# Performance work log

Hardware: AMD Instinct MI355X
Metric: run time of the kernel (lower is better)

The kernel has to match this reference:

```python
import jax, jax.numpy as jnp
import numpy as np

N_NODES = 100000
N_EDGES = 1600000
IN_DIM = 128
HID_DIM = 128


def setup_inputs() -> dict:
    key = jax.random.key(0)
    k_x, k_e, k_w1, k_w2 = jax.random.split(key, 4)
    x = jax.random.normal(k_x, (N_NODES, IN_DIM), dtype=jnp.float32)
    edge_index = jax.random.randint(k_e, (2, N_EDGES), 0, N_NODES, dtype=jnp.int64)
    # Glorot-style init like PyG GCNConv
    s1 = 1.0 / np.sqrt(IN_DIM)
    s2 = 1.0 / np.sqrt(HID_DIM)
    W1 = jax.random.uniform(k_w1, (IN_DIM, HID_DIM), jnp.float32, -s1, s1)
    b1 = jnp.zeros((HID_DIM,), jnp.float32)
    W2 = jax.random.uniform(k_w2, (HID_DIM, HID_DIM), jnp.float32, -s2, s2)
    b2 = jnp.zeros((HID_DIM,), jnp.float32)
    return {"x": x, "edge_index": edge_index, "W1": W1, "b1": b1, "W2": W2, "b2": b2}


def _gcn_norm(edge_index, num_nodes):
    # add self-loops, then symmetric normalization D^{-1/2} (A+I) D^{-1/2}
    loops = jnp.arange(num_nodes, dtype=edge_index.dtype)
    src = jnp.concatenate([edge_index[0], loops])
    dst = jnp.concatenate([edge_index[1], loops])
    deg = jax.ops.segment_sum(jnp.ones_like(dst, dtype=jnp.float32), dst,
                              num_segments=num_nodes)
    dinv = jnp.where(deg > 0, jax.lax.rsqrt(deg), 0.0)
    norm = dinv[src] * dinv[dst]  # [E + N]
    return src, dst, norm


def _gcn_conv(x, W, b, src, dst, norm, num_nodes):
    h = x @ W  # transform first (out_dim == in_dim here, order matches PyG)
    msg = h[src] * norm[:, None]  # gather + scale, [E+N, D]
    out = jax.ops.segment_sum(msg, dst, num_segments=num_nodes)
    return out + b


def reference(x, edge_index, W1, b1, W2, b2):
    n = x.shape[0]
    src, dst, norm = _gcn_norm(edge_index, n)
    h = _gcn_conv(x, W1, b1, src, dst, norm, n)
    h = jax.nn.relu(h)
    return _gcn_conv(h, W2, b2, src, dst, norm, n)
```

## Files before the change

### kernel.cpp

```cpp
#include <hip/hip_runtime.h>
#include <hip/hip_bf16.h>


#define LHSZ 800
#define MAXB 4096
#define CAP  2560

typedef unsigned int uint;
typedef unsigned short ushort;
typedef __attribute__((ext_vector_type(8))) short bf16x8;
typedef __attribute__((ext_vector_type(4))) float f32x4;

static __device__ __forceinline__ float bfl(uint u) { return __uint_as_float(u << 16); }
static __device__ __forceinline__ float bfh(uint u) { return __uint_as_float(u & 0xffff0000u); }
static __device__ __forceinline__ ushort f2bfu(float f) {
    __hip_bfloat16 b = __float2bfloat16(f);
    ushort u; __builtin_memcpy(&u, &b, 2); return u;
}
static __device__ __forceinline__ void splitT(float f, ushort& h, ushort& l) {
    uint u = __float_as_uint(f);
    h = (ushort)(u >> 16);
    float r = f - __uint_as_float(u & 0xffff0000u);
    l = (ushort)(__float_as_uint(r) >> 16);
}

__global__ __launch_bounds__(256) void wsplit_init(
    const float* __restrict__ W1, const float* __restrict__ W2,
    ushort* __restrict__ Ws1, ushort* __restrict__ Ws2,
    int* __restrict__ cur, int nb)
{
    int tg = blockIdx.x * 256 + threadIdx.x;
    int w = tg >> 14;
    int e = tg & 16383;
    int k = e >> 7, n = e & 127;
    float f = (w ? W2 : W1)[e];
    ushort hi, lo; splitT(f, hi, lo);
    int I = (n * 128 + k) ^ ((n & 7) << 3);
    ushort* o = w ? Ws2 : Ws1;
    o[I] = hi; o[I + 16384] = lo;
    if (tg < nb) cur[tg] = tg * CAP;
}

template <int MODE>
static __device__ __forceinline__ void gemm_body(
    ushort* Wt, const void* __restrict__ Ap, const ushort* __restrict__ Wsp,
    ushort* __restrict__ out, int M, int blk)
{
    int t = threadIdx.x;
    {
        const uint4* s4 = (const uint4*)Wsp;
        uint4* d4 = (uint4*)Wt;
        #pragma unroll
        for (int j = 0; j < 16; ++j)
            d4[t + j * 256] = s4[t + j * 256];
    }
    __syncthreads();

    int wv = t >> 6, lane = t & 63;
    int g = lane >> 4;
    int lr = lane & 15;
    int rowbase = blk * 128 + wv * 32;
    int r0 = rowbase + lr, r1 = r0 + 16;
    int rc0 = min(r0, M - 1), rc1 = min(r1, M - 1);

    f32x4 acc[2][8];
    #pragma unroll
    for (int rt = 0; rt < 2; ++rt)
        #pragma unroll
        for (int ct = 0; ct < 8; ++ct)
            acc[rt][ct] = (f32x4)0.0f;

    #pragma unroll
    for (int ks = 0; ks < 4; ++ks) {
        int kof = ks * 32 + g * 8;
        bf16x8 ahi[2], alo[2];
        if (MODE == 0) {
            const float* A = (const float*)Ap;
            #pragma unroll
            for (int rt = 0; rt < 2; ++rt) {
                const float4* p = (const float4*)(A + (size_t)(rt ? rc1 : rc0) * 128 + kof);
                float4 u0 = p[0], u1 = p[1];
                float uu[8] = {u0.x, u0.y, u0.z, u0.w, u1.x, u1.y, u1.z, u1.w};
                bf16x8 ah, al;
                #pragma unroll
                for (int q = 0; q < 8; ++q) {
                    ushort hh, ll; splitT(uu[q], hh, ll);
                    ah[q] = (short)hh; al[q] = (short)ll;
                }
                ahi[rt] = ah; alo[rt] = al;
            }
        } else {
            const ushort* A = (const ushort*)Ap;
            ahi[0] = *(const bf16x8*)(A + (size_t)rc0 * 128 + kof);
            ahi[1] = *(const bf16x8*)(A + (size_t)rc1 * 128 + kof);
        }
        #pragma unroll
        for (int ct = 0; ct < 8; ++ct) {
            int n = ct * 16 + lr;
            int I = (n * 128 + kof) ^ ((n & 7) << 3);
            bf16x8 bhi = *(const bf16x8*)&Wt[I];
            bf16x8 blo = *(const bf16x8*)&Wt[I + 16384];
            #pragma unroll
            for (int rt = 0; rt < 2; ++rt) {
                acc[rt][ct] = __builtin_amdgcn_mfma_f32_16x16x32_bf16(ahi[rt], bhi, acc[rt][ct], 0, 0, 0);
                acc[rt][ct] = __builtin_amdgcn_mfma_f32_16x16x32_bf16(ahi[rt], blo, acc[rt][ct], 0, 0, 0);
                if (MODE == 0)
                    acc[rt][ct] = __builtin_amdgcn_mfma_f32_16x16x32_bf16(alo[rt], bhi, acc[rt][ct], 0, 0, 0);
            }
        }
    }

    #pragma unroll
    for (int rt = 0; rt < 2; ++rt) {
        #pragma unroll
        for (int r = 0; r < 4; ++r) {
            int row = rowbase + rt * 16 + g * 4 + r;
            if (row < M) {
                #pragma unroll
                for (int ct = 0; ct < 8; ++ct)
                    out[(size_t)row * 128 + ct * 16 + lr] = f2bfu(acc[rt][ct][r]);
            }
        }
    }
}

template <int MODE>
__global__ __launch_bounds__(256) void gemm_mfma(
    const void* __restrict__ Ap, const ushort* __restrict__ Wsp,
    ushort* __restrict__ out, int M)
{
    __shared__ ushort Wt[2 * 128 * 128];
    gemm_body<MODE>(Wt, Ap, Wsp, out, M, blockIdx.x);
}

__global__ __launch_bounds__(256) void gemm1_place(
    const float* __restrict__ x, const ushort* __restrict__ Wsp,
    ushort* __restrict__ h, int M, int gemmGrid,
    const int* __restrict__ src, const int* __restrict__ dst,
    int* __restrict__ cur, uint* __restrict__ ppack, int E, int nb, int epb)
{
    __shared__ ushort Wt[2 * 128 * 128];
    if ((int)blockIdx.x >= gemmGrid) {
        int* lhist = (int*)Wt;
        int* gb    = lhist + LHSZ;
        int b = blockIdx.x - gemmGrid;
        int t = threadIdx.x;
        int e0 = b * epb, e1 = min(E, e0 + epb);
        for (int i = t; i < nb; i += 256) lhist[i] = 0;
        __syncthreads();
        for (int e = e0 + t; e < e1; e += 256) atomicAdd(&lhist[dst[e] >> 7], 1);
        __syncthreads();
        for (int i = t; i < nb; i += 256) {
            int v = lhist[i];
            gb[i] = v ? atomicAdd(&cur[i], v) : 0;
            lhist[i] = 0;
        }
        __syncthreads();
        for (int e = e0 + t; e < e1; e += 256) {
            int d = dst[e];
            int b2 = d >> 7;
            int r = atomicAdd(&lhist[b2], 1);
            int pos = gb[b2] + r;
            if (pos < (b2 + 1) * CAP)
                ppack[pos] = (uint)src[e] | ((uint)(d & 127) << 20);
        }
        return;
    }
    gemm_body<0>(Wt, x, Wsp, h, M, blockIdx.x);
}

__global__ __launch_bounds__(256) void csr_finalize(
    const uint* __restrict__ ppack, const int* __restrict__ cur,
    int* __restrict__ csrsrc, uint* __restrict__ meta,
    float* __restrict__ dinv, int N)
{
    __shared__ int ncnt[128], sbuf[128], ncur[128];
    __shared__ int srcbuf[MAXB];
    int t = threadIdx.x;
    int b = blockIdx.x;
    int node0 = b << 7;
    int nn = min(128, N - node0);
    int base = b * CAP;
    int len = min(cur[b] - base, CAP);

    if (t < 128) ncnt[t] = 0;
    __syncthreads();
    for (int i = t; i < len; i += 256)
        atomicAdd(&ncnt[ppack[base + i] >> 20], 1);
    __syncthreads();
    if (t < 128) sbuf[t] = ncnt[t];
    __syncthreads();
    for (int d = 1; d < 128; d <<= 1) {
        int v = 0;
        if (t < 128 && t >= d) v = sbuf[t - d];
        __syncthreads();
        if (t < 128) sbuf[t] += v;
        __syncthreads();
    }
    if (t < 128) {
        int excl = sbuf[t] - ncnt[t];
        ncur[t] = excl;
        if (t < nn) {
            meta[node0 + t] = ((uint)(base + excl) << 10) | (uint)min(ncnt[t], 1023);
            dinv[node0 + t] = rsqrtf((float)(ncnt[t] + 1));
        }
    }
    __syncthreads();
    bool staged = (len <= MAXB);
    for (int i = t; i < len; i += 256) {
        uint p = ppack[base + i];
        int pos = atomicAdd(&ncur[p >> 20], 1);
        int sl = (int)(p & 0xFFFFFu);
        if (staged) srcbuf[pos] = sl;
        else        csrsrc[base + pos] = sl;
    }
    __syncthreads();
    if (staged)
        for (int i = t; i < len; i += 256) csrsrc[base + i] = srcbuf[i];
}

#define FMA4(v, wgt) do { float wf_ = (wgt); \
    acc.x += bfl((v).x) * wf_; acc.y += bfh((v).x) * wf_; \
    acc.z += bfl((v).y) * wf_; acc.w += bfh((v).y) * wf_; } while (0)

template <bool RELU, bool OUTBF>
__global__ __launch_bounds__(256) void agg_kernel(
    const ushort* __restrict__ h, const float* __restrict__ dinv,
    const uint* __restrict__ meta, const int* __restrict__ csrsrc,
    const float* __restrict__ bias, void* __restrict__ outv, int n)
{
    __shared__ int2 epair[4][64];
    int wv = threadIdx.x >> 6;
    int lane = threadIdx.x & 63;
    int half = lane >> 5, sub = lane & 31;
    int node = (blockIdx.x * 4 + wv) * 2 + half;
    bool active = node < n;
    int nodeC = active ? node : (n - 1);

    const uint2* h2 = (const uint2*)h;
    float di = dinv[nodeC];
    uint md = meta[nodeC];
    int beg = (int)(md >> 10);
    int m = (int)(md & 1023u);

    uint2 vs = h2[(size_t)nodeC * 32 + sub];
    float w0 = di * di;
    float4 acc;
    acc.x = bfl(vs.x) * w0; acc.y = bfh(vs.x) * w0;
    acc.z = bfl(vs.y) * w0; acc.w = bfh(vs.y) * w0;

    int mA = __shfl(m, 0), mB = __shfl(m, 32);
    int mmax = max(mA, mB);

    for (int eb = 0; eb < mmax; eb += 32) {
        int sl = 0; float dlw = 0.0f;
        if (active && (eb + sub) < m) {
            sl = csrsrc[beg + eb + sub];
            dlw = di * dinv[sl];
        }
        epair[wv][lane] = make_int2(sl, __float_as_int(dlw));
        int nq = mmax - eb; if (nq > 32) nq = 32;
        const int2* ep = &epair[wv][half * 32];
        for (int j = 0; j < nq; j += 4) {
            int2 p0 = ep[j + 0];
            int2 p1 = ep[j + 1];
            int2 p2 = ep[j + 2];
            int2 p3 = ep[j + 3];
            uint2 v0 = h2[(size_t)(uint)p0.x * 32 + sub];
            uint2 v1 = h2[(size_t)(uint)p1.x * 32 + sub];
            uint2 v2 = h2[(size_t)(uint)p2.x * 32 + sub];
            uint2 v3 = h2[(size_t)(uint)p3.x * 32 + sub];
            FMA4(v0, __int_as_float(p0.y));
            FMA4(v1, __int_as_float(p1.y));
            FMA4(v2, __int_as_float(p2.y));
            FMA4(v3, __int_as_float(p3.y));
        }
    }

    float4 bb = ((const float4*)bias)[sub];
    acc.x += bb.x; acc.y += bb.y; acc.z += bb.z; acc.w += bb.w;
    if (RELU) {
        acc.x = fmaxf(acc.x, 0.0f); acc.y = fmaxf(acc.y, 0.0f);
        acc.z = fmaxf(acc.z, 0.0f); acc.w = fmaxf(acc.w, 0.0f);
    }
    if (active) {
        if (OUTBF) {
            uint2 o;
            o.x = (uint)f2bfu(acc.x) | ((uint)f2bfu(acc.y) << 16);
            o.y = (uint)f2bfu(acc.z) | ((uint)f2bfu(acc.w) << 16);
            ((uint2*)outv)[(size_t)node * 32 + sub] = o;
        } else {
            ((float4*)outv)[(size_t)node * 32 + sub] = acc;
        }
    }
}

extern "C" void kernel_launch(void* const* d_in, const int* in_sizes, int n_in,
                              void* d_out, int out_size, void* d_ws, size_t ws_size,
                              hipStream_t stream)
{
    const float* x  = (const float*)d_in[0];
    const int*   ei = (const int*)d_in[1];
    const float* W1 = (const float*)d_in[2];
    const float* b1 = (const float*)d_in[3];
    const float* W2 = (const float*)d_in[4];
    const float* b2 = (const float*)d_in[5];

    const int N = in_sizes[0] / 128;
    const int E = in_sizes[1] / 2;
    const int* esrc = ei;
    const int* edst = ei + E;
    const int nb = (N + 127) >> 7;

    char* ws = (char*)d_ws;
    size_t off = 0;
    auto alloc = [&](size_t bytes) -> void* {
        void* p = ws + off;
        off += (bytes + 255) & ~(size_t)255;
        return p;
    };
    ushort* h      = (ushort*)alloc((size_t)N * 128 * sizeof(ushort));
    uint*   ppack  = (uint*)  alloc((size_t)nb * CAP * sizeof(uint));
    int*    csrsrc = (int*)   alloc((size_t)nb * CAP * sizeof(int));
    uint*   meta   = (uint*)  alloc((size_t)N * sizeof(uint));
    float*  dinv   = (float*) alloc((size_t)N * sizeof(float));
    int*    cur    = (int*)   alloc((size_t)nb * sizeof(int));
    ushort* Ws1    = (ushort*)alloc(2 * 128 * 128 * sizeof(ushort));
    ushort* Ws2    = (ushort*)alloc(2 * 128 * 128 * sizeof(ushort));

    const int gridP = 512;
    const int epb = (E + gridP - 1) / gridP;
    const int gemmGrid = (N + 127) / 128;

    wsplit_init<<<128, 256, 0, stream>>>(W1, W2, Ws1, Ws2, cur, nb);
    gemm1_place<<<gemmGrid + gridP, 256, 0, stream>>>(x, Ws1, h, N, gemmGrid,
                                                      esrc, edst, cur, ppack,
                                                      E, nb, epb);
    csr_finalize<<<nb, 256, 0, stream>>>(ppack, cur, csrsrc, meta, dinv, N);
    agg_kernel<true, true><<<(N + 7) / 8, 256, 0, stream>>>(h, dinv, meta, csrsrc,
                                                            b1, d_out, N);
    gemm_mfma<1><<<gemmGrid, 256, 0, stream>>>(d_out, Ws2, h, N);
    agg_kernel<false, false><<<(N + 7) / 8, 256, 0, stream>>>(h, dinv, meta, csrsrc,
                                                              b2, d_out, N);
}
```

Baseline: 195.1 us.

## Fuse CSR finalize into aggregation using per-bucket shared-memory edge lists

Removes the separate csr_finalize kernel and the csrsrc/meta/dinv arrays. Each aggregation block of 1024 threads now re-sorts its 128-node bucket from ppack into shared memory and computes per-edge weights from a global degree array. That degree array is built with atomics during the placement pass. This saves a launch and a global CSR round trip, but the bucket sort and the per-edge rsqrt are redone in both aggregation layers, global degree atomics are added, and there is less parallelism per block.

```diff
diff --git a/kernel.cpp b/kernel.cpp
--- a/kernel.cpp
+++ b/kernel.cpp
@@ -3,7 +3,6 @@
 
 
 #define LHSZ 800
-#define MAXB 4096
 #define CAP  2560
 
 typedef unsigned int uint;
@@ -24,10 +23,10 @@
     l = (ushort)(__float_as_uint(r) >> 16);
 }
 
-__global__ __launch_bounds__(256) void wsplit_init(
+__global__ __launch_bounds__(256) void init_all(
     const float* __restrict__ W1, const float* __restrict__ W2,
     ushort* __restrict__ Ws1, ushort* __restrict__ Ws2,
-    int* __restrict__ cur, int nb)
+    int* __restrict__ deg, int* __restrict__ cur, int N, int nb)
 {
     int tg = blockIdx.x * 256 + threadIdx.x;
     int w = tg >> 14;
@@ -38,6 +37,7 @@
     int I = (n * 128 + k) ^ ((n & 7) << 3);
     ushort* o = w ? Ws2 : Ws1;
     o[I] = hi; o[I + 16384] = lo;
+    for (int i = tg; i < N; i += 32768) deg[i] = 0;
     if (tg < nb) cur[tg] = tg * CAP;
 }
 
@@ -137,7 +137,8 @@
     const float* __restrict__ x, const ushort* __restrict__ Wsp,
     ushort* __restrict__ h, int M, int gemmGrid,
     const int* __restrict__ src, const int* __restrict__ dst,
-    int* __restrict__ cur, uint* __restrict__ ppack, int E, int nb, int epb)
+    int* __restrict__ cur, int* __restrict__ deg,
+    uint* __restrict__ ppack, int E, int nb, int epb)
 {
     __shared__ ushort Wt[2 * 128 * 128];
     if ((int)blockIdx.x >= gemmGrid) {
@@ -148,7 +149,11 @@
         int e0 = b * epb, e1 = min(E, e0 + epb);
         for (int i = t; i < nb; i += 256) lhist[i] = 0;
         __syncthreads();
-        for (int e = e0 + t; e < e1; e += 256) atomicAdd(&lhist[dst[e] >> 7], 1);
+        for (int e = e0 + t; e < e1; e += 256) {
+            int d = dst[e];
+            atomicAdd(&lhist[d >> 7], 1);
+            atomicAdd(&deg[d], 1);
+        }
         __syncthreads();
         for (int i = t; i < nb; i += 256) {
             int v = lhist[i];
@@ -169,24 +174,34 @@
     gemm_body<0>(Wt, x, Wsp, h, M, blockIdx.x);
 }
 
-__global__ __launch_bounds__(256) void csr_finalize(
+#define FMA4(v, wgt) do { float wf_ = (wgt); \
+    acc.x += bfl((v).x) * wf_; acc.y += bfh((v).x) * wf_; \
+    acc.z += bfl((v).y) * wf_; acc.w += bfh((v).y) * wf_; } while (0)
+
+template <bool RELU, bool OUTBF>
+__global__ __launch_bounds__(1024) void agg_fused(
+    const ushort* __restrict__ h, const int* __restrict__ deg,
     const uint* __restrict__ ppack, const int* __restrict__ cur,
-    int* __restrict__ csrsrc, uint* __restrict__ meta,
-    float* __restrict__ dinv, int N)
-{
+    const float* __restrict__ bias, void* __restrict__ outv, int n)
+{
+    __shared__ int   lsrc[CAP];
+    __shared__ float lwt[CAP];
     __shared__ int ncnt[128], sbuf[128], ncur[128];
-    __shared__ int srcbuf[MAXB];
+    __shared__ float dloc[128];
     int t = threadIdx.x;
     int b = blockIdx.x;
     int node0 = b << 7;
-    int nn = min(128, N - node0);
     int base = b * CAP;
     int len = min(cur[b] - base, CAP);
 
     if (t < 128) ncnt[t] = 0;
     __syncthreads();
-    for (int i = t; i < len; i += 256)
-        atomicAdd(&ncnt[ppack[base + i] >> 20], 1);
+    uint myp[3]; int mc = 0;
+    for (int i = t; i < len; i += 1024) {
+        uint p = ppack[base + i];
+        myp[mc++] = p;
+        atomicAdd(&ncnt[p >> 20], 1);
+    }
     __syncthreads();
     if (t < 128) sbuf[t] = ncnt[t];
     __syncthreads();
@@ -198,99 +213,75 @@
         __syncthreads();
     }
     if (t < 128) {
-        int excl = sbuf[t] - ncnt[t];
-        ncur[t] = excl;
-        if (t < nn) {
-            meta[node0 + t] = ((uint)(base + excl) << 10) | (uint)min(ncnt[t], 1023);
-            dinv[node0 + t] = rsqrtf((float)(ncnt[t] + 1));
-        }
-    }
-    __syncthreads();
-    bool staged = (len <= MAXB);
-    for (int i = t; i < len; i += 256) {
-        uint p = ppack[base + i];
+        ncur[t] = sbuf[t] - ncnt[t];
+        dloc[t] = rsqrtf((float)(ncnt[t] + 1));
+    }
+    __syncthreads();
+    for (int k = 0; k < mc; ++k) {
+        uint p = myp[k];
         int pos = atomicAdd(&ncur[p >> 20], 1);
-        int sl = (int)(p & 0xFFFFFu);
-        if (staged) srcbuf[pos] = sl;
-        else        csrsrc[base + pos] = sl;
-    }
-    __syncthreads();
-    if (staged)
-        for (int i = t; i < len; i += 256) csrsrc[base + i] = srcbuf[i];
-}
-
-#define FMA4(v, wgt) do { float wf_ = (wgt); \
-    acc.x += bfl((v).x) * wf_; acc.y += bfh((v).x) * wf_; \
-    acc.z += bfl((v).y) * wf_; acc.w += bfh((v).y) * wf_; } while (0)
-
-template <bool RELU, bool OUTBF>
-__global__ __launch_bounds__(256) void agg_kernel(
-    const ushort* __restrict__ h, const float* __restrict__ dinv,
-    const uint* __restrict__ meta, const int* __restrict__ csrsrc,
-    const float* __restrict__ bias, void* __restrict__ outv, int n)
-{
-    __shared__ int2 epair[4][64];
-    int wv = threadIdx.x >> 6;
-    int lane = threadIdx.x & 63;
+        lsrc[pos] = (int)(p & 0xFFFFFu);
+    }
+    __syncthreads();
+    for (int i = t; i < len; i += 1024)
+        lwt[i] = rsqrtf((float)(deg[lsrc[i]] + 1));
+    __syncthreads();
+
+    int wv = t >> 6, lane = t & 63;
     int half = lane >> 5, sub = lane & 31;
-    int node = (blockIdx.x * 4 + wv) * 2 + half;
-    bool active = node < n;
-    int nodeC = active ? node : (n - 1);
-
     const uint2* h2 = (const uint2*)h;
-    float di = dinv[nodeC];
-    uint md = meta[nodeC];
-    int beg = (int)(md >> 10);
-    int m = (int)(md & 1023u);
-
-    uint2 vs = h2[(size_t)nodeC * 32 + sub];
-    float w0 = di * di;
-    float4 acc;
-    acc.x = bfl(vs.x) * w0; acc.y = bfh(vs.x) * w0;
-    acc.z = bfl(vs.y) * w0; acc.w = bfh(vs.y) * w0;
-
-    int mA = __shfl(m, 0), mB = __shfl(m, 32);
-    int mmax = max(mA, mB);
-
-    for (int eb = 0; eb < mmax; eb += 32) {
-        int sl = 0; float dlw = 0.0f;
-        if (active && (eb + sub) < m) {
-            sl = csrsrc[beg + eb + sub];
-            dlw = di * dinv[sl];
-        }
-        epair[wv][lane] = make_int2(sl, __float_as_int(dlw));
-        int nq = mmax - eb; if (nq > 32) nq = 32;
-        const int2* ep = &epair[wv][half * 32];
-        for (int j = 0; j < nq; j += 4) {
-            int2 p0 = ep[j + 0];
-            int2 p1 = ep[j + 1];
-            int2 p2 = ep[j + 2];
-            int2 p3 = ep[j + 3];
-            uint2 v0 = h2[(size_t)(uint)p0.x * 32 + sub];
-            uint2 v1 = h2[(size_t)(uint)p1.x * 32 + sub];
-            uint2 v2 = h2[(size_t)(uint)p2.x * 32 + sub];
-            uint2 v3 = h2[(size_t)(uint)p3.x * 32 + sub];
-            FMA4(v0, __int_as_float(p0.y));
-            FMA4(v1, __int_as_float(p1.y));
-            FMA4(v2, __int_as_float(p2.y));
-            FMA4(v3, __int_as_float(p3.y));
-        }
-    }
-
-    float4 bb = ((const float4*)bias)[sub];
-    acc.x += bb.x; acc.y += bb.y; acc.z += bb.z; acc.w += bb.w;
-    if (RELU) {
-        acc.x = fmaxf(acc.x, 0.0f); acc.y = fmaxf(acc.y, 0.0f);
-        acc.z = fmaxf(acc.z, 0.0f); acc.w = fmaxf(acc.w, 0.0f);
-    }
-    if (active) {
-        if (OUTBF) {
-            uint2 o;
-            o.x = (uint)f2bfu(acc.x) | ((uint)f2bfu(acc.y) << 16);
-            o.y = (uint)f2bfu(acc.z) | ((uint)f2bfu(acc.w) << 16);
-            ((uint2*)outv)[(size_t)node * 32 + sub] = o;
-        } else {
-            ((float4*)outv)[(size_t)node * 32 + sub] = acc;
+
+    for (int pp = 0; pp < 4; ++pp) {
+        int ln = pp * 32 + wv * 2 + half;
+        int node = node0 + ln;
+        bool active = node < n;
+        int nodeC = active ? node : (n - 1);
+        float di = dloc[ln];
+        int m = ncnt[ln];
+        int beg = ncur[ln] - m;
+
+        uint2 vs = h2[(size_t)nodeC * 32 + sub];
+        float4 acc = make_float4(0.0f, 0.0f, 0.0f, 0.0f);
+
+        int j = 0;
+        for (; j + 4 <= m; j += 4) {
+            int s0 = lsrc[beg + j + 0], s1 = lsrc[beg + j + 1];
+            int s2 = lsrc[beg + j + 2], s3 = lsrc[beg + j + 3];
+            float q0 = lwt[beg + j + 0], q1 = lwt[beg + j + 1];
+            float q2 = lwt[beg + j + 2], q3 = lwt[beg + j + 3];
+            uint2 v0 = h2[(size_t)(uint)s0 * 32 + sub];
+            uint2 v1 = h2[(size_t)(uint)s1 * 32 + sub];
+            uint2 v2 = h2[(size_t)(uint)s2 * 32 + sub];
+            uint2 v3 = h2[(size_t)(uint)s3 * 32 + sub];
+            FMA4(v0, q0); FMA4(v1, q1); FMA4(v2, q2); FMA4(v3, q3);
+        }
+        for (; j < m; ++j) {
+            int s0 = lsrc[beg + j];
+            float q0 = lwt[beg + j];
+            uint2 v0 = h2[(size_t)(uint)s0 * 32 + sub];
+            FMA4(v0, q0);
+        }
+
+        float w0 = di * di;
+        acc.x = acc.x * di + bfl(vs.x) * w0;
+        acc.y = acc.y * di + bfh(vs.x) * w0;
+        acc.z = acc.z * di + bfl(vs.y) * w0;
+        acc.w = acc.w * di + bfh(vs.y) * w0;
+        float4 bb = ((const float4*)bias)[sub];
+        acc.x += bb.x; acc.y += bb.y; acc.z += bb.z; acc.w += bb.w;
+        if (RELU) {
+            acc.x = fmaxf(acc.x, 0.0f); acc.y = fmaxf(acc.y, 0.0f);
+            acc.z = fmaxf(acc.z, 0.0f); acc.w = fmaxf(acc.w, 0.0f);
+        }
+        if (active) {
+            if (OUTBF) {
+                uint2 o;
+                o.x = (uint)f2bfu(acc.x) | ((uint)f2bfu(acc.y) << 16);
+                o.y = (uint)f2bfu(acc.z) | ((uint)f2bfu(acc.w) << 16);
+                ((uint2*)outv)[(size_t)node * 32 + sub] = o;
+            } else {
+                ((float4*)outv)[(size_t)node * 32 + sub] = acc;
+            }
         }
     }
 }
@@ -321,9 +312,7 @@
     };
     ushort* h      = (ushort*)alloc((size_t)N * 128 * sizeof(ushort));
     uint*   ppack  = (uint*)  alloc((size_t)nb * CAP * sizeof(uint));
-    int*    csrsrc = (int*)   alloc((size_t)nb * CAP * sizeof(int));
-    uint*   meta   = (uint*)  alloc((size_t)N * sizeof(uint));
-    float*  dinv   = (float*) alloc((size_t)N * sizeof(float));
+    int*    deg    = (int*)   alloc((size_t)N * sizeof(int));
     int*    cur    = (int*)   alloc((size_t)nb * sizeof(int));
     ushort* Ws1    = (ushort*)alloc(2 * 128 * 128 * sizeof(ushort));
     ushort* Ws2    = (ushort*)alloc(2 * 128 * 128 * sizeof(ushort));
@@ -332,14 +321,13 @@
     const int epb = (E + gridP - 1) / gridP;
     const int gemmGrid = (N + 127) / 128;
 
-    wsplit_init<<<128, 256, 0, stream>>>(W1, W2, Ws1, Ws2, cur, nb);
+    init_all<<<128, 256, 0, stream>>>(W1, W2, Ws1, Ws2, deg, cur, N, nb);
     gemm1_place<<<gemmGrid + gridP, 256, 0, stream>>>(x, Ws1, h, N, gemmGrid,
-                                                      esrc, edst, cur, ppack,
-                                                      E, nb, epb);
-    csr_finalize<<<nb, 256, 0, stream>>>(ppack, cur, csrsrc, meta, dinv, N);
-    agg_kernel<true, true><<<(N + 7) / 8, 256, 0, stream>>>(h, dinv, meta, csrsrc,
-                                                            b1, d_out, N);
+                                                      esrc, edst, cur, deg,
+                                                      ppack, E, nb, epb);
+    agg_fused<true, true><<<nb, 1024, 0, stream>>>(h, deg, ppack, cur,
+                                                   b1, d_out, N);
     gemm_mfma<1><<<gemmGrid, 256, 0, stream>>>(d_out, Ws2, h, N);
-    agg_kernel<false, false><<<(N + 7) / 8, 256, 0, stream>>>(h, dinv, meta, csrsrc,
-                                                              b2, d_out, N);
-}
+    agg_fused<false, false><<<nb, 1024, 0, stream>>>(h, deg, ppack, cur,
+                                                     b2, d_out, N);
+}
```

After: 271.9 us. 39.4% more time.

## Co-schedule CSR finalize with first GEMM instead of bucket placement

Applied to the files above, without the earlier changes.

Moves edge bucket placement into its own small kernel and merges the CSR finalize step into the first GEMM launch as extra blocks. The finalize blocks then overlap with GEMM blocks rather than running as a separate serial launch. Placement loses its overlap with the GEMM, and finalize blocks now occupy the GEMM kernel's 64KB LDS allocation, which may lower occupancy for those blocks.

```diff
diff --git a/kernel.cpp b/kernel.cpp
--- a/kernel.cpp
+++ b/kernel.cpp
@@ -39,6 +39,85 @@
     ushort* o = w ? Ws2 : Ws1;
     o[I] = hi; o[I + 16384] = lo;
     if (tg < nb) cur[tg] = tg * CAP;
+}
+
+__global__ __launch_bounds__(256) void bucket_place(
+    const int* __restrict__ src, const int* __restrict__ dst,
+    int* __restrict__ cur, uint* __restrict__ ppack, int E, int nb, int epb)
+{
+    __shared__ int lhist[LHSZ];
+    __shared__ int gb[LHSZ];
+    int t = threadIdx.x;
+    int e0 = blockIdx.x * epb, e1 = min(E, e0 + epb);
+    for (int i = t; i < nb; i += 256) lhist[i] = 0;
+    __syncthreads();
+    for (int e = e0 + t; e < e1; e += 256) atomicAdd(&lhist[dst[e] >> 7], 1);
+    __syncthreads();
+    for (int i = t; i < nb; i += 256) {
+        int v = lhist[i];
+        gb[i] = v ? atomicAdd(&cur[i], v) : 0;
+        lhist[i] = 0;
+    }
+    __syncthreads();
+    for (int e = e0 + t; e < e1; e += 256) {
+        int d = dst[e];
+        int b2 = d >> 7;
+        int r = atomicAdd(&lhist[b2], 1);
+        int pos = gb[b2] + r;
+        if (pos < (b2 + 1) * CAP)
+            ppack[pos] = (uint)src[e] | ((uint)(d & 127) << 20);
+    }
+}
+
+static __device__ __forceinline__ void finalize_body(
+    char* lds, const uint* __restrict__ ppack, const int* __restrict__ cur,
+    int* __restrict__ csrsrc, uint* __restrict__ meta,
+    float* __restrict__ dinv, int N, int b)
+{
+    int* ncnt  = (int*)lds;
+    int* sbuf  = ncnt + 128;
+    int* ncur  = sbuf + 128;
+    int* srcbuf = ncur + 128;
+    int t = threadIdx.x;
+    int node0 = b << 7;
+    int nn = min(128, N - node0);
+    int base = b * CAP;
+    int len = min(cur[b] - base, CAP);
+
+    if (t < 128) ncnt[t] = 0;
+    __syncthreads();
+    for (int i = t; i < len; i += 256)
+        atomicAdd(&ncnt[ppack[base + i] >> 20], 1);
+    __syncthreads();
+    if (t < 128) sbuf[t] = ncnt[t];
+    __syncthreads();
+    for (int d = 1; d < 128; d <<= 1) {
+        int v = 0;
+        if (t < 128 && t >= d) v = sbuf[t - d];
+        __syncthreads();
+        if (t < 128) sbuf[t] += v;
+        __syncthreads();
+    }
+    if (t < 128) {
+        int excl = sbuf[t] - ncnt[t];
+        ncur[t] = excl;
+        if (t < nn) {
+            meta[node0 + t] = ((uint)(base + excl) << 10) | (uint)min(ncnt[t], 1023);
+            dinv[node0 + t] = rsqrtf((float)(ncnt[t] + 1));
+        }
+    }
+    __syncthreads();
+    bool staged = (len <= MAXB);
+    for (int i = t; i < len; i += 256) {
+        uint p = ppack[base + i];
+        int pos = atomicAdd(&ncur[p >> 20], 1);
+        int sl = (int)(p & 0xFFFFFu);
+        if (staged) srcbuf[pos] = sl;
+        else        csrsrc[base + pos] = sl;
+    }
+    __syncthreads();
+    if (staged)
+        for (int i = t; i < len; i += 256) csrsrc[base + i] = srcbuf[i];
 }
 
 template <int MODE>
@@ -133,90 +212,20 @@
     gemm_body<MODE>(Wt, Ap, Wsp, out, M, blockIdx.x);
 }
 
-__global__ __launch_bounds__(256) void gemm1_place(
+__global__ __launch_bounds__(256) void gemm1_fin(
     const float* __restrict__ x, const ushort* __restrict__ Wsp,
     ushort* __restrict__ h, int M, int gemmGrid,
-    const int* __restrict__ src, const int* __restrict__ dst,
-    int* __restrict__ cur, uint* __restrict__ ppack, int E, int nb, int epb)
-{
-    __shared__ ushort Wt[2 * 128 * 128];
-    if ((int)blockIdx.x >= gemmGrid) {
-        int* lhist = (int*)Wt;
-        int* gb    = lhist + LHSZ;
-        int b = blockIdx.x - gemmGrid;
-        int t = threadIdx.x;
-        int e0 = b * epb, e1 = min(E, e0 + epb);
-        for (int i = t; i < nb; i += 256) lhist[i] = 0;
-        __syncthreads();
-        for (int e = e0 + t; e < e1; e += 256) atomicAdd(&lhist[dst[e] >> 7], 1);
-        __syncthreads();
-        for (int i = t; i < nb; i += 256) {
-            int v = lhist[i];
-            gb[i] = v ? atomicAdd(&cur[i], v) : 0;
-            lhist[i] = 0;
-        }
-        __syncthreads();
-        for (int e = e0 + t; e < e1; e += 256) {
-            int d = dst[e];
-            int b2 = d >> 7;
-            int r = atomicAdd(&lhist[b2], 1);
-            int pos = gb[b2] + r;
-            if (pos < (b2 + 1) * CAP)
-                ppack[pos] = (uint)src[e] | ((uint)(d & 127) << 20);
-        }
-        return;
-    }
-    gemm_body<0>(Wt, x, Wsp, h, M, blockIdx.x);
-}
-
-__global__ __launch_bounds__(256) void csr_finalize(
     const uint* __restrict__ ppack, const int* __restrict__ cur,
     int* __restrict__ csrsrc, uint* __restrict__ meta,
     float* __restrict__ dinv, int N)
 {
-    __shared__ int ncnt[128], sbuf[128], ncur[128];
-    __shared__ int srcbuf[MAXB];
-    int t = threadIdx.x;
-    int b = blockIdx.x;
-    int node0 = b << 7;
-    int nn = min(128, N - node0);
-    int base = b * CAP;
-    int len = min(cur[b] - base, CAP);
-
-    if (t < 128) ncnt[t] = 0;
-    __syncthreads();
-    for (int i = t; i < len; i += 256)
-        atomicAdd(&ncnt[ppack[base + i] >> 20], 1);
-    __syncthreads();
-    if (t < 128) sbuf[t] = ncnt[t];
-    __syncthreads();
-    for (int d = 1; d < 128; d <<= 1) {
-        int v = 0;
-        if (t < 128 && t >= d) v = sbuf[t - d];
-        __syncthreads();
-        if (t < 128) sbuf[t] += v;
-        __syncthreads();
-    }
-    if (t < 128) {
-        int excl = sbuf[t] - ncnt[t];
-        ncur[t] = excl;
-        if (t < nn) {
-            meta[node0 + t] = ((uint)(base + excl) << 10) | (uint)min(ncnt[t], 1023);
-            dinv[node0 + t] = rsqrtf((float)(ncnt[t] + 1));
-        }
-    }
-    __syncthreads();
-    bool staged = (len <= MAXB);
-    for (int i = t; i < len; i += 256) {
-        uint p = ppack[base + i];
-        int pos = atomicAdd(&ncur[p >> 20], 1);
-        int sl = (int)(p & 0xFFFFFu);
-        if (staged) srcbuf[pos] = sl;
-        else        csrsrc[base + pos] = sl;
-    }
-    __syncthreads();
-    if (staged)
-        for (int i = t; i < len; i += 256) csrsrc[base + i] = srcbuf[i];
+    __shared__ ushort Wt[2 * 128 * 128];
+    if ((int)blockIdx.x >= gemmGrid) {
+        finalize_body((char*)Wt, ppack, cur, csrsrc, meta, dinv, N,
+                      blockIdx.x - gemmGrid);
+        return;
+    }
+    gemm_body<0>(Wt, x, Wsp, h, M, blockIdx.x);
 }
 
 #define FMA4(v, wgt) do { float wf_ = (wgt); \
@@ -333,10 +342,10 @@
     const int gemmGrid = (N + 127) / 128;
 
     wsplit_init<<<128, 256, 0, stream>>>(W1, W2, Ws1, Ws2, cur, nb);
-    gemm1_place<<<gemmGrid + gridP, 256, 0, stream>>>(x, Ws1, h, N, gemmGrid,
-                                                      esrc, edst, cur, ppack,
-                                                      E, nb, epb);
-    csr_finalize<<<nb, 256, 0, stream>>>(ppack, cur, csrsrc, meta, dinv, N);
+    bucket_place<<<gridP, 256, 0, stream>>>(esrc, edst, cur, ppack, E, nb, epb);
+    gemm1_fin<<<gemmGrid + nb, 256, 0, stream>>>(x, Ws1, h, N, gemmGrid,
+                                                 ppack, cur, csrsrc, meta,
+                                                 dinv, N);
     agg_kernel<true, true><<<(N + 7) / 8, 256, 0, stream>>>(h, dinv, meta, csrsrc,
                                                             b1, d_out, N);
     gemm_mfma<1><<<gemmGrid, 256, 0, stream>>>(d_out, Ws2, h, N);
```

New measurement: 208.0 us. +6.6%, slower.

## Store hidden features in 16-column slices to shrink the gather footprint

Applied to the files above, without the earlier changes.

The GEMM now writes the bf16 hidden matrix in a sliced layout, eight slabs of N×16 columns, and the second GEMM reads that same layout. Aggregation becomes a slice kernel: each block handles one 16-column slice for 64 nodes, with 4 threads per node looping over that node's CSR neighbours. The goal is a per-slice gather working set small enough to stay in cache. The cost is that each neighbour's index and dinv are re-read by every slice and for each of the 4 lanes, and edge loops can diverge across nodes of different degree. Normalisation is restructured so di is applied once at the end.

```diff
diff --git a/kernel.cpp b/kernel.cpp
--- a/kernel.cpp
+++ b/kernel.cpp
@@ -91,8 +91,9 @@
             }
         } else {
             const ushort* A = (const ushort*)Ap;
-            ahi[0] = *(const bf16x8*)(A + (size_t)rc0 * 128 + kof);
-            ahi[1] = *(const bf16x8*)(A + (size_t)rc1 * 128 + kof);
+            int sl = kof >> 4, of = kof & 15;
+            ahi[0] = *(const bf16x8*)(A + ((size_t)sl * M + rc0) * 16 + of);
+            ahi[1] = *(const bf16x8*)(A + ((size_t)sl * M + rc1) * 16 + of);
         }
         #pragma unroll
         for (int ct = 0; ct < 8; ++ct) {
@@ -118,7 +119,7 @@
             if (row < M) {
                 #pragma unroll
                 for (int ct = 0; ct < 8; ++ct)
-                    out[(size_t)row * 128 + ct * 16 + lr] = f2bfu(acc[rt][ct][r]);
+                    out[((size_t)ct * M + row) * 16 + lr] = f2bfu(acc[rt][ct][r]);
             }
         }
     }
@@ -224,74 +225,62 @@
     acc.z += bfl((v).y) * wf_; acc.w += bfh((v).y) * wf_; } while (0)
 
 template <bool RELU, bool OUTBF>
-__global__ __launch_bounds__(256) void agg_kernel(
-    const ushort* __restrict__ h, const float* __restrict__ dinv,
+__global__ __launch_bounds__(256) void agg_slice(
+    const ushort* __restrict__ hs, const float* __restrict__ dinv,
     const uint* __restrict__ meta, const int* __restrict__ csrsrc,
     const float* __restrict__ bias, void* __restrict__ outv, int n)
 {
-    __shared__ int2 epair[4][64];
-    int wv = threadIdx.x >> 6;
-    int lane = threadIdx.x & 63;
-    int half = lane >> 5, sub = lane & 31;
-    int node = (blockIdx.x * 4 + wv) * 2 + half;
-    bool active = node < n;
-    int nodeC = active ? node : (n - 1);
-
-    const uint2* h2 = (const uint2*)h;
-    float di = dinv[nodeC];
-    uint md = meta[nodeC];
+    int t = threadIdx.x;
+    int s = blockIdx.x & 7;
+    int node = (blockIdx.x >> 3) * 64 + (t >> 2);
+    int f = t & 3;
+    if (node >= n) return;
+
+    const uint2* h2 = (const uint2*)hs + (size_t)s * n * 4;
+    float di = dinv[node];
+    uint md = meta[node];
     int beg = (int)(md >> 10);
     int m = (int)(md & 1023u);
 
-    uint2 vs = h2[(size_t)nodeC * 32 + sub];
-    float w0 = di * di;
-    float4 acc;
-    acc.x = bfl(vs.x) * w0; acc.y = bfh(vs.x) * w0;
-    acc.z = bfl(vs.y) * w0; acc.w = bfh(vs.y) * w0;
-
-    int mA = __shfl(m, 0), mB = __shfl(m, 32);
-    int mmax = max(mA, mB);
-
-    for (int eb = 0; eb < mmax; eb += 32) {
-        int sl = 0; float dlw = 0.0f;
-        if (active && (eb + sub) < m) {
-            sl = csrsrc[beg + eb + sub];
-            dlw = di * dinv[sl];
-        }
-        epair[wv][lane] = make_int2(sl, __float_as_int(dlw));
-        int nq = mmax - eb; if (nq > 32) nq = 32;
-        const int2* ep = &epair[wv][half * 32];
-        for (int j = 0; j < nq; j += 4) {
-            int2 p0 = ep[j + 0];
-            int2 p1 = ep[j + 1];
-            int2 p2 = ep[j + 2];
-            int2 p3 = ep[j + 3];
-            uint2 v0 = h2[(size_t)(uint)p0.x * 32 + sub];
-            uint2 v1 = h2[(size_t)(uint)p1.x * 32 + sub];
-            uint2 v2 = h2[(size_t)(uint)p2.x * 32 + sub];
-            uint2 v3 = h2[(size_t)(uint)p3.x * 32 + sub];
-            FMA4(v0, __int_as_float(p0.y));
-            FMA4(v1, __int_as_float(p1.y));
-            FMA4(v2, __int_as_float(p2.y));
-            FMA4(v3, __int_as_float(p3.y));
-        }
-    }
-
-    float4 bb = ((const float4*)bias)[sub];
+    uint2 vs = h2[(size_t)node * 4 + f];
+    float4 acc = make_float4(0.0f, 0.0f, 0.0f, 0.0f);
+
+    int j = 0;
+    for (; j + 4 <= m; j += 4) {
+        int s0 = csrsrc[beg + j + 0], s1 = csrsrc[beg + j + 1];
+        int s2 = csrsrc[beg + j + 2], s3 = csrsrc[beg + j + 3];
+        float w0 = dinv[s0], w1 = dinv[s1], w2 = dinv[s2], w3 = dinv[s3];
+        uint2 v0 = h2[(size_t)(uint)s0 * 4 + f];
+        uint2 v1 = h2[(size_t)(uint)s1 * 4 + f];
+        uint2 v2 = h2[(size_t)(uint)s2 * 4 + f];
+        uint2 v3 = h2[(size_t)(uint)s3 * 4 + f];
+        FMA4(v0, w0); FMA4(v1, w1); FMA4(v2, w2); FMA4(v3, w3);
+    }
+    for (; j < m; ++j) {
+        int s0 = csrsrc[beg + j];
+        float w0 = dinv[s0];
+        uint2 v0 = h2[(size_t)(uint)s0 * 4 + f];
+        FMA4(v0, w0);
+    }
+
+    float sw = di * di;
+    acc.x = acc.x * di + bfl(vs.x) * sw;
+    acc.y = acc.y * di + bfh(vs.x) * sw;
+    acc.z = acc.z * di + bfl(vs.y) * sw;
+    acc.w = acc.w * di + bfh(vs.y) * sw;
+    float4 bb = ((const float4*)bias)[s * 4 + f];
     acc.x += bb.x; acc.y += bb.y; acc.z += bb.z; acc.w += bb.w;
     if (RELU) {
         acc.x = fmaxf(acc.x, 0.0f); acc.y = fmaxf(acc.y, 0.0f);
         acc.z = fmaxf(acc.z, 0.0f); acc.w = fmaxf(acc.w, 0.0f);
     }
-    if (active) {
-        if (OUTBF) {
-            uint2 o;
-            o.x = (uint)f2bfu(acc.x) | ((uint)f2bfu(acc.y) << 16);
-            o.y = (uint)f2bfu(acc.z) | ((uint)f2bfu(acc.w) << 16);
-            ((uint2*)outv)[(size_t)node * 32 + sub] = o;
-        } else {
-            ((float4*)outv)[(size_t)node * 32 + sub] = acc;
-        }
+    if (OUTBF) {
+        uint2 o;
+        o.x = (uint)f2bfu(acc.x) | ((uint)f2bfu(acc.y) << 16);
+        o.y = (uint)f2bfu(acc.z) | ((uint)f2bfu(acc.w) << 16);
+        ((uint2*)outv)[((size_t)s * n + node) * 4 + f] = o;
+    } else {
+        ((float4*)outv)[(size_t)node * 32 + s * 4 + f] = acc;
     }
 }
 
@@ -331,15 +320,16 @@
     const int gridP = 512;
     const int epb = (E + gridP - 1) / gridP;
     const int gemmGrid = (N + 127) / 128;
+    const int aggGrid = 8 * ((N + 63) / 64);
 
     wsplit_init<<<128, 256, 0, stream>>>(W1, W2, Ws1, Ws2, cur, nb);
     gemm1_place<<<gemmGrid + gridP, 256, 0, stream>>>(x, Ws1, h, N, gemmGrid,
                                                       esrc, edst, cur, ppack,
                                                       E, nb, epb);
     csr_finalize<<<nb, 256, 0, stream>>>(ppack, cur, csrsrc, meta, dinv, N);
-    agg_kernel<true, true><<<(N + 7) / 8, 256, 0, stream>>>(h, dinv, meta, csrsrc,
-                                                            b1, d_out, N);
+    agg_slice<true, true><<<aggGrid, 256, 0, stream>>>(h, dinv, meta, csrsrc,
+                                                       b1, d_out, N);
     gemm_mfma<1><<<gemmGrid, 256, 0, stream>>>(d_out, Ws2, h, N);
-    agg_kernel<false, false><<<(N + 7) / 8, 256, 0, stream>>>(h, dinv, meta, csrsrc,
-                                                              b2, d_out, N);
-}
+    agg_slice<false, false><<<aggGrid, 256, 0, stream>>>(h, dinv, meta, csrsrc,
+                                                         b2, d_out, N);
+}
```

Measured after the change: 347.6 us. +78.2%, slower.
